# Optimization experiments

Hardware: AMD Instinct MI355X
Metric: run time of the kernel (lower is better)

## Reference

```python
import jax, jax.numpy as jnp
import numpy as np

EMBED = 1024
HEADS = 16
HEAD_DIM = EMBED // HEADS


def setup_inputs() -> dict:
    key = jax.random.key(0)
    ks = jax.random.split(key, 12)
    B, S = 2, 2048
    inp = {
        'v': jax.random.normal(ks[0], (B, S, EMBED), jnp.float32),
        'k': jax.random.normal(ks[1], (B, S, EMBED), jnp.float32),
        'q': jax.random.normal(ks[2], (B, S, EMBED), jnp.float32),
        'mask': jnp.ones((B, 1, S, S), dtype=bool),
        'Wv': jax.random.normal(ks[3], (EMBED, EMBED), jnp.float32) * 0.02,
        'bv': jax.random.normal(ks[4], (EMBED,), jnp.float32) * 0.02,
        'Wk': jax.random.normal(ks[5], (EMBED, EMBED), jnp.float32) * 0.02,
        'bk': jax.random.normal(ks[6], (EMBED,), jnp.float32) * 0.02,
        'Wq': jax.random.normal(ks[7], (EMBED, EMBED), jnp.float32) * 0.02,
        'bq': jax.random.normal(ks[8], (EMBED,), jnp.float32) * 0.02,
        'Wo': jax.random.normal(ks[9], (EMBED, EMBED), jnp.float32) * 0.02,
        'bo': jax.random.normal(ks[10], (EMBED,), jnp.float32) * 0.02,
    }
    return inp


def reference(v, k, q, mask, Wv, bv, Wk, bk, Wq, bq, Wo, bo):
    N, q_len, _ = q.shape
    k_len = k.shape[1]
    # linear projections (torch Linear: x @ W.T + b)
    vh = (v @ Wv.T + bv).reshape(N, -1, HEADS, HEAD_DIM)
    kh = (k @ Wk.T + bk).reshape(N, k_len, HEADS, HEAD_DIM)
    qh = (q @ Wq.T + bq).reshape(N, q_len, HEADS, HEAD_DIM)
    # scores [N, H, q, k]
    energy = jnp.einsum('nqhd,nkhd->nhqk', qh, kh)
    # NOTE: original masks BEFORE dividing by sqrt(embed_size)
    energy = jnp.where(mask, energy, jnp.float32(-1e20))
    attention = jax.nn.softmax(energy / jnp.sqrt(jnp.float32(EMBED)), axis=3)
    out = jnp.einsum('nhqk,nkhd->nqhd', attention, vh).reshape(N, q_len, EMBED)
    return out @ Wo.T + bo
```

## Files before the change

### kernel.cpp

```cpp
#include <hip/hip_runtime.h>
#include <cstdint>
#include <cstddef>


typedef uint16_t u16;
typedef uint32_t u32;
typedef unsigned long long u64;
using bf16x8 = __attribute__((ext_vector_type(8))) __bf16;
using bf16x2 = __attribute__((ext_vector_type(2))) __bf16;
using f32x4  = __attribute__((ext_vector_type(4))) float;
using f32x16 = __attribute__((ext_vector_type(16))) float;
using u16x8  = __attribute__((ext_vector_type(8))) uint16_t;
using u16x4  = __attribute__((ext_vector_type(4))) uint16_t;
using u32x4  = __attribute__((ext_vector_type(4))) uint32_t;

#define S_LEN 2048
#define EMB   1024
#define NHEAD 16
#define HDIM  64
#define BATCH 2
#define MROWS (BATCH * S_LEN)
#define NBITW (BATCH * S_LEN * (S_LEN / 64))

__device__ __forceinline__ u16 f2bf(float f) {
  uint32_t u = __float_as_uint(f);
  u += 0x7FFFu + ((u >> 16) & 1u);
  return (u16)(u >> 16);
}

__device__ __forceinline__ float fexp2(float x) {
#if __has_builtin(__builtin_amdgcn_exp2f)
  return __builtin_amdgcn_exp2f(x);
#else
  return exp2f(x);
#endif
}

__device__ __forceinline__ u32 packbf(float a, float b) {
  bf16x2 v = { (__bf16)a, (__bf16)b };
  return __builtin_bit_cast(u32, v);
}

__device__ __forceinline__ void async16(void* lds, const void* g) {
  __builtin_amdgcn_global_load_lds(
      (const __attribute__((address_space(1))) void*)g,
      (__attribute__((address_space(3))) void*)lds, 16, 0, 0);
}

__global__ __launch_bounds__(256) void mask_compact(const uint32_t* __restrict__ m,
                                                    u64* __restrict__ bits) {
  const int i = blockIdx.x * 256 + threadIdx.x;
  if (i >= NBITW) return;
  const bool bytew = (m[0] == 0x01010101u);
  u64 b = 0;
  if (bytew) {
    const uint32_t* src = m + (size_t)i * 16;
#pragma unroll
    for (int w = 0; w < 16; ++w) {
      const uint32_t v = src[w];
#pragma unroll
      for (int j = 0; j < 4; ++j)
        b |= (u64)(((v >> (8 * j)) & 0xFFu) != 0u) << (w * 4 + j);
    }
  } else {
    const uint32_t* src = m + (size_t)i * 64;
#pragma unroll
    for (int j = 0; j < 64; ++j) b |= (u64)(src[j] != 0u) << j;
  }
  bits[i] = b;
}

struct ConvArgs {
  const float* src[7];
  u16* dst[7];
  int n4[7];
};

__global__ __launch_bounds__(256) void convert_bf16(ConvArgs a) {
  const int j = blockIdx.y;
  const float4* s = (const float4*)a.src[j];
  u16* d = a.dst[j];
  const int n4 = a.n4[j];
  for (int i = blockIdx.x * 256 + threadIdx.x; i < n4; i += gridDim.x * 256) {
    float4 v = s[i];
    u16x4 o = { f2bf(v.x), f2bf(v.y), f2bf(v.z), f2bf(v.w) };
    *(u16x4*)(d + (size_t)i * 4) = o;
  }
}

template <typename OutT>
__device__ __forceinline__ void gemm_body(const u16* __restrict__ A,
                                          const u16* __restrict__ W,
                                          const float* __restrict__ bias,
                                          OutT* __restrict__ C, float scale) {
  constexpr int K = 1024, N = 1024;
  __shared__ alignas(16) u16 As[128 * 32];
  __shared__ alignas(16) u16 Bs[128 * 32];
  const int t = threadIdx.x;
  const int wave = t >> 6, lane = t & 63;
  const int wr = wave >> 1, wc = wave & 1;
  const int m0 = blockIdx.y * 128, n0 = blockIdx.x * 128;
  f32x4 acc[4][4] = {};
  const int srow = wave * 16 + (lane >> 2);
  const int soff = (lane & 3) * 8;
  const u16* gA = A + (size_t)(m0 + srow) * K + soff;
  const u16* gB = W + (size_t)(n0 + srow) * K + soff;
  u16* lA = As + wave * 512;
  u16* lB = Bs + wave * 512;
  const int fo = (lane >> 4) * 8;
  const int fr = lane & 15;

  for (int kt = 0; kt < K; kt += 32) {
    async16(lA,        gA + kt);
    async16(lA + 2048, gA + (size_t)64 * K + kt);
    async16(lB,        gB + kt);
    async16(lB + 2048, gB + (size_t)64 * K + kt);
    __syncthreads();
    bf16x8 af[4], bfr[4];
#pragma unroll
    for (int i = 0; i < 4; ++i)
      af[i] = *(const bf16x8*)(As + (wr * 64 + i * 16 + fr) * 32 + fo);
#pragma unroll
    for (int i = 0; i < 4; ++i)
      bfr[i] = *(const bf16x8*)(Bs + (wc * 64 + i * 16 + fr) * 32 + fo);
#pragma unroll
    for (int mi = 0; mi < 4; ++mi)
#pragma unroll
      for (int ni = 0; ni < 4; ++ni)
        acc[mi][ni] = __builtin_amdgcn_mfma_f32_16x16x32_bf16(af[mi], bfr[ni],
                                                              acc[mi][ni], 0, 0, 0);
    __syncthreads();
  }
  const int r0 = (lane >> 4) * 4;
#pragma unroll
  for (int mi = 0; mi < 4; ++mi) {
    const int rowb = m0 + wr * 64 + mi * 16 + r0;
#pragma unroll
    for (int ni = 0; ni < 4; ++ni) {
      const int col = n0 + wc * 64 + ni * 16 + fr;
      const float bv = bias[col];
#pragma unroll
      for (int r = 0; r < 4; ++r) {
        float v = (acc[mi][ni][r] + bv) * scale;
        if constexpr (sizeof(OutT) == 2)
          C[(size_t)(rowb + r) * N + col] = f2bf(v);
        else
          C[(size_t)(rowb + r) * N + col] = v;
      }
    }
  }
}

struct ProjArgs {
  const u16* A[3];
  const u16* W[3];
  const float* bias[3];
  u16* C[3];
  float scale[3];
};

__global__ __launch_bounds__(256) void gemm_proj3(ProjArgs p) {
  const int z = blockIdx.z;
  gemm_body<u16>(p.A[z], p.W[z], p.bias[z], p.C[z], p.scale[z]);
}

__global__ __launch_bounds__(256) void gemm_out(const u16* __restrict__ A,
                                                const u16* __restrict__ W,
                                                const float* __restrict__ bias,
                                                float* __restrict__ C) {
  gemm_body<float>(A, W, bias, C, 1.0f);
}

__global__ __launch_bounds__(256, 2) void attn_fa(const u16* __restrict__ Qh,
                                                  const u16* __restrict__ Kh,
                                                  const u16* __restrict__ Vh,
                                                  const u64* __restrict__ mbits,
                                                  u16* __restrict__ O) {
  __shared__ alignas(16) u16 Kt[2][64 * 64];
  __shared__ alignas(16) u16 Vt[2][64 * 64];
  const int t = threadIdx.x, wave = t >> 6, lane = t & 63;
  const int b = blockIdx.y >> 4, h = blockIdx.y & 15;
  const int ql = lane & 31;
  const int hi = lane >> 5;
  const int qrow = blockIdx.x * 128 + wave * 32 + ql;

  const u16* qbase = Qh + (size_t)(b * S_LEN + qrow) * EMB + h * HDIM + hi * 8;
  bf16x8 qf[4];
#pragma unroll
  for (int dk = 0; dk < 4; ++dk)
    qf[dk] = *(const bf16x8*)(qbase + dk * 16);

  const int srow = t >> 3;
  const int schunk = t & 7;
  const u16* kbase = Kh + (size_t)(b * S_LEN) * EMB + h * HDIM;
  const u16* vbase = Vh + (size_t)(b * S_LEN) * EMB + h * HDIM;
  const int vdg = t & 7, vkp = t >> 3;
  const int vd0 = vdg * 8, vk0 = vkp * 2;

  u16x8 va, vb;
  {
    async16(&Kt[0][0] + wave * 512,
            kbase + (size_t)srow * EMB + ((schunk ^ (srow & 7)) * 8));
    async16(&Kt[0][0] + 2048 + wave * 512,
            kbase + (size_t)(srow + 32) * EMB + ((schunk ^ ((srow + 32) & 7)) * 8));
    const u16* vs = vbase + (size_t)vk0 * EMB + vd0;
    va = *(const u16x8*)vs;
    vb = *(const u16x8*)(vs + EMB);
  }
#pragma unroll
  for (int j = 0; j < 8; ++j) {
    const int d = vd0 + j;
    const u32 val = (u32)va[j] | ((u32)vb[j] << 16);
    *(u32*)((char*)&Vt[0][0] + (d * 128 + ((vkp * 4) ^ ((d & 7) << 4)))) = val;
  }
  __syncthreads();

  f32x16 o[2] = {};
  float mreg = -1.0e30f, lloc = 0.f;
  const u64* mword = mbits + (size_t)(b * S_LEN + qrow) * 32;

  for (int kt = 0; kt < 32; ++kt) {
    const int cur = kt & 1, nxt = cur ^ 1;
    if (kt < 31) {
      const int kvn = (kt + 1) * 64;
      async16(&Kt[nxt][0] + wave * 512,
              kbase + (size_t)(kvn + srow) * EMB + ((schunk ^ (srow & 7)) * 8));
      async16(&Kt[nxt][0] + 2048 + wave * 512,
              kbase + (size_t)(kvn + srow + 32) * EMB +
                  ((schunk ^ ((srow + 32) & 7)) * 8));
      const u16* vs = vbase + (size_t)(kvn + vk0) * EMB + vd0;
      va = *(const u16x8*)vs;
      vb = *(const u16x8*)(vs + EMB);
    }

    f32x16 s[2] = {};
#pragma unroll
    for (int kb = 0; kb < 2; ++kb) {
      const int key = kb * 32 + ql;
      const char* kRow = (const char*)&Kt[cur][0] + key * 128;
#pragma unroll
      for (int dk = 0; dk < 4; ++dk) {
        const bf16x8 kf =
            *(const bf16x8*)(kRow + ((dk * 32 + hi * 16) ^ ((key & 7) << 4)));
        s[kb] = __builtin_amdgcn_mfma_f32_32x32x16_bf16(kf, qf[dk], s[kb], 0, 0, 0);
      }
    }

    const u64 mw = mword[kt];
    if (!__all((int)(mw == ~0ull))) {
#pragma unroll
      for (int kb = 0; kb < 2; ++kb)
#pragma unroll
        for (int r = 0; r < 16; ++r) {
          const int key = 32 * kb + (r & 3) + 8 * (r >> 2) + 4 * hi;
          if (!((mw >> key) & 1ull)) s[kb][r] = -1.0e20f;
        }
    }

    float tm = s[0][0];
#pragma unroll
    for (int kb = 0; kb < 2; ++kb)
#pragma unroll
      for (int r = 0; r < 16; ++r) tm = fmaxf(tm, s[kb][r]);
    tm = fmaxf(tm, __shfl_xor(tm, 32));
    if (!__all((int)(tm <= mreg + 8.0f))) {
      const float mn = fmaxf(mreg, tm);
      const float al = fexp2(mreg - mn);
      mreg = mn;
      lloc *= al;
#pragma unroll
      for (int dB = 0; dB < 2; ++dB)
#pragma unroll
        for (int r = 0; r < 16; ++r) o[dB][r] *= al;
    }
    float ts = 0.f;
#pragma unroll
    for (int kb = 0; kb < 2; ++kb)
#pragma unroll
      for (int r = 0; r < 16; ++r) {
        const float p = fexp2(s[kb][r] - mreg);
        s[kb][r] = p;
        ts += p;
      }
    lloc += ts;

    u32 w[2][8], pw[2][8];
#pragma unroll
    for (int kb = 0; kb < 2; ++kb)
#pragma unroll
      for (int i = 0; i < 8; ++i) {
        w[kb][i] = packbf(s[kb][2 * i], s[kb][2 * i + 1]);
        pw[kb][i] = (u32)__shfl_xor((int)w[kb][i], 32);
      }
    const bool hiL = (hi != 0);
    bf16x8 pf[4];
#pragma unroll
    for (int ks = 0; ks < 4; ++ks) {
      const int kb = ks >> 1, iL = (ks & 1) * 4;
      const u32 a0 = hiL ? pw[kb][iL + 2] : w[kb][iL + 0];
      const u32 a1 = hiL ? pw[kb][iL + 3] : w[kb][iL + 1];
      const u32 a2 = hiL ? w[kb][iL + 2] : pw[kb][iL + 0];
      const u32 a3 = hiL ? w[kb][iL + 3] : pw[kb][iL + 1];
      const u32x4 uv = {a0, a1, a2, a3};
      pf[ks] = __builtin_bit_cast(bf16x8, uv);
    }

#pragma unroll
    for (int dB = 0; dB < 2; ++dB) {
      const int d = dB * 32 + ql;
      const char* vRow = (const char*)&Vt[cur][0] + d * 128;
#pragma unroll
      for (int ks = 0; ks < 4; ++ks) {
        const bf16x8 vf =
            *(const bf16x8*)(vRow + ((ks * 32 + hi * 16) ^ ((d & 7) << 4)));
        o[dB] = __builtin_amdgcn_mfma_f32_32x32x16_bf16(vf, pf[ks], o[dB], 0, 0, 0);
      }
    }

    if (kt < 31) {
#pragma unroll
      for (int j = 0; j < 8; ++j) {
        const int d = vd0 + j;
        const u32 val = (u32)va[j] | ((u32)vb[j] << 16);
        *(u32*)((char*)&Vt[nxt][0] + (d * 128 + ((vkp * 4) ^ ((d & 7) << 4)))) = val;
      }
    }
    __syncthreads();
  }

  const float inv = 1.0f / (lloc + __shfl_xor(lloc, 32));
  u16* ob = O + (size_t)(b * S_LEN + qrow) * EMB + h * HDIM;
#pragma unroll
  for (int dB = 0; dB < 2; ++dB)
#pragma unroll
    for (int rr = 0; rr < 4; ++rr) {
      u16x4 st;
#pragma unroll
      for (int m = 0; m < 4; ++m) st[m] = f2bf(o[dB][rr * 4 + m] * inv);
      *(u16x4*)(ob + dB * 32 + rr * 8 + hi * 4) = st;
    }
}

extern "C" void kernel_launch(void* const* d_in, const int* in_sizes, int n_in,
                              void* d_out, int out_size, void* d_ws, size_t ws_size,
                              hipStream_t stream) {
  const float* v_in = (const float*)d_in[0];
  const float* k_in = (const float*)d_in[1];
  const float* q_in = (const float*)d_in[2];
  const uint32_t* mask = (const uint32_t*)d_in[3];
  const float* Wv = (const float*)d_in[4];
  const float* bv = (const float*)d_in[5];
  const float* Wk = (const float*)d_in[6];
  const float* bk = (const float*)d_in[7];
  const float* Wq = (const float*)d_in[8];
  const float* bq = (const float*)d_in[9];
  const float* Wo = (const float*)d_in[10];
  const float* bo = (const float*)d_in[11];

  char* ws = (char*)d_ws;
  const size_t SZX = (size_t)MROWS * EMB * 2;
  const size_t SZW = (size_t)EMB * EMB * 2;
  u16* qh  = (u16*)(ws);
  u16* kh  = (u16*)(ws + SZX);
  u16* vh  = (u16*)(ws + 2 * SZX);
  u16* Obf = (u16*)(ws + 3 * SZX);
  u16* Wqb = (u16*)(ws + 4 * SZX);
  u16* Wkb = (u16*)(ws + 4 * SZX + SZW);
  u16* Wvb = (u16*)(ws + 4 * SZX + 2 * SZW);
  u16* Wob = (u16*)(ws + 4 * SZX + 3 * SZW);
  u16* qbf = (u16*)(ws + 4 * SZX + 4 * SZW);
  u16* kbf = (u16*)(ws + 5 * SZX + 4 * SZW);
  u16* vbf = (u16*)(ws + 6 * SZX + 4 * SZW);
  u64* mbits = (u64*)(ws + 7 * SZX + 4 * SZW);

  mask_compact<<<dim3(NBITW / 256), 256, 0, stream>>>(mask, mbits);

  ConvArgs ca;
  ca.src[0] = q_in; ca.dst[0] = qbf; ca.n4[0] = MROWS * EMB / 4;
  ca.src[1] = k_in; ca.dst[1] = kbf; ca.n4[1] = MROWS * EMB / 4;
  ca.src[2] = v_in; ca.dst[2] = vbf; ca.n4[2] = MROWS * EMB / 4;
  ca.src[3] = Wq;   ca.dst[3] = Wqb; ca.n4[3] = EMB * EMB / 4;
  ca.src[4] = Wk;   ca.dst[4] = Wkb; ca.n4[4] = EMB * EMB / 4;
  ca.src[5] = Wv;   ca.dst[5] = Wvb; ca.n4[5] = EMB * EMB / 4;
  ca.src[6] = Wo;   ca.dst[6] = Wob; ca.n4[6] = EMB * EMB / 4;
  convert_bf16<<<dim3(256, 7), 256, 0, stream>>>(ca);

  ProjArgs pa;
  const float qscale = 1.4426950408889634f / 32.0f;
  pa.A[0] = qbf; pa.W[0] = Wqb; pa.bias[0] = bq; pa.C[0] = qh; pa.scale[0] = qscale;
  pa.A[1] = kbf; pa.W[1] = Wkb; pa.bias[1] = bk; pa.C[1] = kh; pa.scale[1] = 1.0f;
  pa.A[2] = vbf; pa.W[2] = Wvb; pa.bias[2] = bv; pa.C[2] = vh; pa.scale[2] = 1.0f;
  gemm_proj3<<<dim3(8, 32, 3), 256, 0, stream>>>(pa);

  attn_fa<<<dim3(S_LEN / 128, BATCH * NHEAD), 256, 0, stream>>>(qh, kh, vh, mbits, Obf);

  gemm_out<<<dim3(8, 32), 256, 0, stream>>>(Obf, Wob, bo, (float*)d_out);
}
```

Baseline: 157.4 us.

## Retile output GEMM, change LDS swizzle, use permlane32 swap for P

```diff
diff --git a/kernel.cpp b/kernel.cpp
--- a/kernel.cpp
+++ b/kernel.cpp
@@ -41,6 +41,10 @@
   return __builtin_bit_cast(u32, v);
 }
 
+__device__ __forceinline__ void plswap(u32& a, u32& b) {
+  asm volatile("v_permlane32_swap_b32 %0, %1" : "+v"(a), "+v"(b));
+}
+
 __device__ __forceinline__ void async16(void* lds, const void* g) {
   __builtin_amdgcn_global_load_lds(
       (const __attribute__((address_space(1))) void*)g,
@@ -88,19 +92,19 @@
   }
 }
 
-template <typename OutT>
+template <int BM, int BN, int FM, int FN, typename OutT>
 __device__ __forceinline__ void gemm_body(const u16* __restrict__ A,
                                           const u16* __restrict__ W,
                                           const float* __restrict__ bias,
                                           OutT* __restrict__ C, float scale) {
   constexpr int K = 1024, N = 1024;
-  __shared__ alignas(16) u16 As[128 * 32];
-  __shared__ alignas(16) u16 Bs[128 * 32];
+  __shared__ alignas(16) u16 As[BM * 32];
+  __shared__ alignas(16) u16 Bs[BN * 32];
   const int t = threadIdx.x;
   const int wave = t >> 6, lane = t & 63;
   const int wr = wave >> 1, wc = wave & 1;
-  const int m0 = blockIdx.y * 128, n0 = blockIdx.x * 128;
-  f32x4 acc[4][4] = {};
+  const int m0 = blockIdx.y * BM, n0 = blockIdx.x * BN;
+  f32x4 acc[FM][FN] = {};
   const int srow = wave * 16 + (lane >> 2);
   const int soff = (lane & 3) * 8;
   const u16* gA = A + (size_t)(m0 + srow) * K + soff;
@@ -111,33 +115,35 @@
   const int fr = lane & 15;
 
   for (int kt = 0; kt < K; kt += 32) {
-    async16(lA,        gA + kt);
-    async16(lA + 2048, gA + (size_t)64 * K + kt);
-    async16(lB,        gB + kt);
-    async16(lB + 2048, gB + (size_t)64 * K + kt);
+#pragma unroll
+    for (int a = 0; a < BM / 64; ++a)
+      async16(lA + a * 2048, gA + (size_t)(a * 64) * K + kt);
+#pragma unroll
+    for (int a = 0; a < BN / 64; ++a)
+      async16(lB + a * 2048, gB + (size_t)(a * 64) * K + kt);
     __syncthreads();
-    bf16x8 af[4], bfr[4];
-#pragma unroll
-    for (int i = 0; i < 4; ++i)
-      af[i] = *(const bf16x8*)(As + (wr * 64 + i * 16 + fr) * 32 + fo);
-#pragma unroll
-    for (int i = 0; i < 4; ++i)
-      bfr[i] = *(const bf16x8*)(Bs + (wc * 64 + i * 16 + fr) * 32 + fo);
-#pragma unroll
-    for (int mi = 0; mi < 4; ++mi)
-#pragma unroll
-      for (int ni = 0; ni < 4; ++ni)
+    bf16x8 af[FM], bfr[FN];
+#pragma unroll
+    for (int i = 0; i < FM; ++i)
+      af[i] = *(const bf16x8*)(As + (wr * (FM * 16) + i * 16 + fr) * 32 + fo);
+#pragma unroll
+    for (int i = 0; i < FN; ++i)
+      bfr[i] = *(const bf16x8*)(Bs + (wc * (FN * 16) + i * 16 + fr) * 32 + fo);
+#pragma unroll
+    for (int mi = 0; mi < FM; ++mi)
+#pragma unroll
+      for (int ni = 0; ni < FN; ++ni)
         acc[mi][ni] = __builtin_amdgcn_mfma_f32_16x16x32_bf16(af[mi], bfr[ni],
                                                               acc[mi][ni], 0, 0, 0);
     __syncthreads();
   }
   const int r0 = (lane >> 4) * 4;
 #pragma unroll
-  for (int mi = 0; mi < 4; ++mi) {
-    const int rowb = m0 + wr * 64 + mi * 16 + r0;
-#pragma unroll
-    for (int ni = 0; ni < 4; ++ni) {
-      const int col = n0 + wc * 64 + ni * 16 + fr;
+  for (int mi = 0; mi < FM; ++mi) {
+    const int rowb = m0 + wr * (FM * 16) + mi * 16 + r0;
+#pragma unroll
+    for (int ni = 0; ni < FN; ++ni) {
+      const int col = n0 + wc * (FN * 16) + ni * 16 + fr;
       const float bv = bias[col];
 #pragma unroll
       for (int r = 0; r < 4; ++r) {
@@ -161,14 +167,14 @@
 
 __global__ __launch_bounds__(256) void gemm_proj3(ProjArgs p) {
   const int z = blockIdx.z;
-  gemm_body<u16>(p.A[z], p.W[z], p.bias[z], p.C[z], p.scale[z]);
+  gemm_body<128, 128, 4, 4, u16>(p.A[z], p.W[z], p.bias[z], p.C[z], p.scale[z]);
 }
 
 __global__ __launch_bounds__(256) void gemm_out(const u16* __restrict__ A,
                                                 const u16* __restrict__ W,
                                                 const float* __restrict__ bias,
                                                 float* __restrict__ C) {
-  gemm_body<float>(A, W, bias, C, 1.0f);
+  gemm_body<64, 128, 2, 4, float>(A, W, bias, C, 1.0f);
 }
 
 __global__ __launch_bounds__(256, 2) void attn_fa(const u16* __restrict__ Qh,
@@ -192,17 +198,20 @@
 
   const int srow = t >> 3;
   const int schunk = t & 7;
+  const int fk0 = (srow + (srow >> 3)) & 7;
+  const int fk1 = (srow + 32 + ((srow + 32) >> 3)) & 7;
   const u16* kbase = Kh + (size_t)(b * S_LEN) * EMB + h * HDIM;
   const u16* vbase = Vh + (size_t)(b * S_LEN) * EMB + h * HDIM;
   const int vdg = t & 7, vkp = t >> 3;
   const int vd0 = vdg * 8, vk0 = vkp * 2;
+  const int vg_hi = (vkp >> 2) & 7, vg_lo = (vkp & 3) * 4;
 
   u16x8 va, vb;
   {
     async16(&Kt[0][0] + wave * 512,
-            kbase + (size_t)srow * EMB + ((schunk ^ (srow & 7)) * 8));
+            kbase + (size_t)srow * EMB + ((schunk ^ fk0) * 8));
     async16(&Kt[0][0] + 2048 + wave * 512,
-            kbase + (size_t)(srow + 32) * EMB + ((schunk ^ ((srow + 32) & 7)) * 8));
+            kbase + (size_t)(srow + 32) * EMB + ((schunk ^ fk1) * 8));
     const u16* vs = vbase + (size_t)vk0 * EMB + vd0;
     va = *(const u16x8*)vs;
     vb = *(const u16x8*)(vs + EMB);
@@ -210,8 +219,9 @@
 #pragma unroll
   for (int j = 0; j < 8; ++j) {
     const int d = vd0 + j;
+    const int fd = (d + (d >> 3)) & 7;
     const u32 val = (u32)va[j] | ((u32)vb[j] << 16);
-    *(u32*)((char*)&Vt[0][0] + (d * 128 + ((vkp * 4) ^ ((d & 7) << 4)))) = val;
+    *(u32*)((char*)&Vt[0][0] + (d * 128 + ((vg_hi ^ fd) << 4) + vg_lo)) = val;
   }
   __syncthreads();
 
@@ -224,10 +234,9 @@
     if (kt < 31) {
       const int kvn = (kt + 1) * 64;
       async16(&Kt[nxt][0] + wave * 512,
-              kbase + (size_t)(kvn + srow) * EMB + ((schunk ^ (srow & 7)) * 8));
+              kbase + (size_t)(kvn + srow) * EMB + ((schunk ^ fk0) * 8));
       async16(&Kt[nxt][0] + 2048 + wave * 512,
-              kbase + (size_t)(kvn + srow + 32) * EMB +
-                  ((schunk ^ ((srow + 32) & 7)) * 8));
+              kbase + (size_t)(kvn + srow + 32) * EMB + ((schunk ^ fk1) * 8));
       const u16* vs = vbase + (size_t)(kvn + vk0) * EMB + vd0;
       va = *(const u16x8*)vs;
       vb = *(const u16x8*)(vs + EMB);
@@ -237,11 +246,12 @@
 #pragma unroll
     for (int kb = 0; kb < 2; ++kb) {
       const int key = kb * 32 + ql;
+      const int fkk = (key + (key >> 3)) & 7;
       const char* kRow = (const char*)&Kt[cur][0] + key * 128;
 #pragma unroll
       for (int dk = 0; dk < 4; ++dk) {
         const bf16x8 kf =
-            *(const bf16x8*)(kRow + ((dk * 32 + hi * 16) ^ ((key & 7) << 4)));
+            *(const bf16x8*)(kRow + (((dk * 2 + hi) ^ fkk) << 4));
         s[kb] = __builtin_amdgcn_mfma_f32_32x32x16_bf16(kf, qf[dk], s[kb], 0, 0, 0);
       }
     }
@@ -284,35 +294,36 @@
       }
     lloc += ts;
 
-    u32 w[2][8], pw[2][8];
-#pragma unroll
-    for (int kb = 0; kb < 2; ++kb)
-#pragma unroll
-      for (int i = 0; i < 8; ++i) {
-        w[kb][i] = packbf(s[kb][2 * i], s[kb][2 * i + 1]);
-        pw[kb][i] = (u32)__shfl_xor((int)w[kb][i], 32);
-      }
-    const bool hiL = (hi != 0);
     bf16x8 pf[4];
 #pragma unroll
-    for (int ks = 0; ks < 4; ++ks) {
-      const int kb = ks >> 1, iL = (ks & 1) * 4;
-      const u32 a0 = hiL ? pw[kb][iL + 2] : w[kb][iL + 0];
-      const u32 a1 = hiL ? pw[kb][iL + 3] : w[kb][iL + 1];
-      const u32 a2 = hiL ? w[kb][iL + 2] : pw[kb][iL + 0];
-      const u32 a3 = hiL ? w[kb][iL + 3] : pw[kb][iL + 1];
-      const u32x4 uv = {a0, a1, a2, a3};
-      pf[ks] = __builtin_bit_cast(bf16x8, uv);
+    for (int kb = 0; kb < 2; ++kb) {
+      u32 w0 = packbf(s[kb][0], s[kb][1]);
+      u32 w1 = packbf(s[kb][2], s[kb][3]);
+      u32 w2 = packbf(s[kb][4], s[kb][5]);
+      u32 w3 = packbf(s[kb][6], s[kb][7]);
+      u32 w4 = packbf(s[kb][8], s[kb][9]);
+      u32 w5 = packbf(s[kb][10], s[kb][11]);
+      u32 w6 = packbf(s[kb][12], s[kb][13]);
+      u32 w7 = packbf(s[kb][14], s[kb][15]);
+      plswap(w0, w2);
+      plswap(w1, w3);
+      plswap(w4, w6);
+      plswap(w5, w7);
+      const u32x4 lo = {w0, w1, w2, w3};
+      const u32x4 hi4 = {w4, w5, w6, w7};
+      pf[kb * 2 + 0] = __builtin_bit_cast(bf16x8, lo);
+      pf[kb * 2 + 1] = __builtin_bit_cast(bf16x8, hi4);
     }
 
 #pragma unroll
     for (int dB = 0; dB < 2; ++dB) {
       const int d = dB * 32 + ql;
+      const int fd = (d + (d >> 3)) & 7;
       const char* vRow = (const char*)&Vt[cur][0] + d * 128;
 #pragma unroll
       for (int ks = 0; ks < 4; ++ks) {
         const bf16x8 vf =
-            *(const bf16x8*)(vRow + ((ks * 32 + hi * 16) ^ ((d & 7) << 4)));
+            *(const bf16x8*)(vRow + (((ks * 2 + hi) ^ fd) << 4));
         o[dB] = __builtin_amdgcn_mfma_f32_32x32x16_bf16(vf, pf[ks], o[dB], 0, 0, 0);
       }
     }
@@ -321,8 +332,9 @@
 #pragma unroll
       for (int j = 0; j < 8; ++j) {
         const int d = vd0 + j;
+        const int fd = (d + (d >> 3)) & 7;
         const u32 val = (u32)va[j] | ((u32)vb[j] << 16);
-        *(u32*)((char*)&Vt[nxt][0] + (d * 128 + ((vkp * 4) ^ ((d & 7) << 4)))) = val;
+        *(u32*)((char*)&Vt[nxt][0] + (d * 128 + ((vg_hi ^ fd) << 4) + vg_lo)) = val;
       }
     }
     __syncthreads();
@@ -394,5 +406,5 @@
 
   attn_fa<<<dim3(S_LEN / 128, BATCH * NHEAD), 256, 0, stream>>>(qh, kh, vh, mbits, Obf);
 
-  gemm_out<<<dim3(8, 32), 256, 0, stream>>>(Obf, Wob, bo, (float*)d_out);
-}
+  gemm_out<<<dim3(8, 64), 256, 0, stream>>>(Obf, Wob, bo, (float*)d_out);
+}
```

Result: faster. 142.3 us (-9.6%).
